# Kernel optimization log

Hardware: AMD Instinct MI355X
Metric: run time of the kernel (lower is better)

## Reference

```python
import jax, jax.numpy as jnp
import numpy as np

N = 50000
F_IN = 512
H = 256
L = 52
E = 1600000


def gcn_conv(x, W, b, src, dst):
    """PyG GCNConv: add self-loops, symmetric norm D^-1/2 (A+I) D^-1/2, then X W + b.
    src/dst already include self-loops."""
    h = x @ W  # [N, H]
    deg = jax.ops.segment_sum(jnp.ones_like(dst, dtype=h.dtype), dst, num_segments=N)
    dinv = jnp.where(deg > 0, jax.lax.rsqrt(deg), 0.0)
    w = dinv[src] * dinv[dst]  # [E+N]
    out = jax.ops.segment_sum(h[src] * w[:, None], dst, num_segments=N)
    return out + b


def _branch(x, src, dst, params):
    (W1, b1), (W2, b2), (W3, b3), (We, be) = params
    x = jax.nn.relu(gcn_conv(x, W1, b1, src, dst))
    x = jax.nn.relu(gcn_conv(x, W2, b2, src, dst))
    x = jax.nn.relu(gcn_conv(x, W3, b3, src, dst))
    return gcn_conv(x, We, be, src, dst)


def setup_inputs() -> dict:
    key = jax.random.key(0)
    ks = jax.random.split(key, 32)
    d = {}
    d["x_1"] = jax.random.normal(ks[0], (N, F_IN), dtype=jnp.float32)
    d["x_2"] = jax.random.normal(ks[1], (N, F_IN), dtype=jnp.float32)
    d["edge_index_1"] = jax.random.randint(ks[2], (2, E), 0, N, dtype=jnp.int32)
    d["edge_index_2"] = jax.random.randint(ks[3], (2, E), 0, N, dtype=jnp.int32)

    def lin(k, fi, fo):
        s = 1.0 / np.sqrt(fi)
        return jax.random.uniform(k, (fi, fo), jnp.float32, -s, s)

    i = 4
    for br in (1, 2):
        fis = [F_IN, H, H, H]
        for li, nm in enumerate(["1", "2", "3", "e"]):
            d[f"Wc{nm}{br}"] = lin(ks[i], fis[li], H); i += 1
            d[f"bc{nm}{br}"] = jnp.zeros((H,), jnp.float32)
    d["w1_W"] = lin(ks[i], H, 1); i += 1
    d["w1_b"] = jnp.zeros((1,), jnp.float32)
    d["w2_W"] = lin(ks[i], H, 1); i += 1
    d["w2_b"] = jnp.zeros((1,), jnp.float32)
    d["fin_W"] = lin(ks[i], H, H); i += 1
    d["fin_b"] = jnp.zeros((H,), jnp.float32)
    d["out_W"] = lin(ks[i], H, L); i += 1
    d["out_b"] = jnp.zeros((L,), jnp.float32)
    return d


def reference(x_1, edge_index_1, x_2, edge_index_2,
              Wc11, bc11, Wc21, bc21, Wc31, bc31, Wce1, bce1,
              Wc12, bc12, Wc22, bc22, Wc32, bc32, Wce2, bce2,
              w1_W, w1_b, w2_W, w2_b, fin_W, fin_b, out_W, out_b):
    loop = jnp.arange(N)
    s1 = jnp.concatenate([edge_index_1[0], loop])
    d1 = jnp.concatenate([edge_index_1[1], loop])
    s2 = jnp.concatenate([edge_index_2[0], loop])
    d2 = jnp.concatenate([edge_index_2[1], loop])

    h1 = _branch(x_1, s1, d1, [(Wc11, bc11), (Wc21, bc21), (Wc31, bc31), (Wce1, bce1)])
    h2 = _branch(x_2, s2, d2, [(Wc12, bc12), (Wc22, bc22), (Wc32, bc32), (Wce2, bce2)])

    f1 = jax.nn.sigmoid(h1 @ w1_W + w1_b)  # [N,1]
    f2 = jax.nn.sigmoid(h2 @ w2_W + w2_b)
    f1 = f1 / (f1 + f2)
    out = f1 * h1 + (1.0 - f1) * h2
    out = jax.nn.relu(out @ fin_W + fin_b)
    return jax.nn.sigmoid(out @ out_W + out_b)
```

## Files before the change

kernel.cpp:

```cpp
#include <hip/hip_runtime.h>
#include <math.h>

#define N_NODES 50000
#define F_IN    512
#define HDIM    256
#define L_OUT   52
#define E_EDGES 1600000

typedef short short8 __attribute__((ext_vector_type(8)));
typedef unsigned short u16x8 __attribute__((ext_vector_type(8)));
typedef float f32x4 __attribute__((ext_vector_type(4)));
typedef float f32x2 __attribute__((ext_vector_type(2)));

__device__ __forceinline__ float bf2f(unsigned short u) {
    unsigned int x = ((unsigned int)u) << 16;
    return __builtin_bit_cast(float, x);
}
__device__ __forceinline__ unsigned short f2bf(float f) {
    unsigned int u = __builtin_bit_cast(unsigned int, f);
    return (unsigned short)((u + 0x7fffu + ((u >> 16) & 1u)) >> 16);
}
__device__ __forceinline__ unsigned char f2fp8(float f) {
    int pk = __builtin_amdgcn_cvt_pk_fp8_f32(f, 0.f, 0, false);
    return (unsigned char)(pk & 0xff);
}
__device__ __forceinline__ void gload16(const unsigned short* g, unsigned short* l) {
    __builtin_amdgcn_global_load_lds(
        (const __attribute__((address_space(1))) unsigned int*)(g),
        (__attribute__((address_space(3))) unsigned int*)(l), 16, 0, 0);
}


__global__ void k_rank2(const int* __restrict__ d1, const int* __restrict__ d2,
                        int* __restrict__ c1, int* __restrict__ c2,
                        int* __restrict__ rk1, int* __restrict__ rk2, int E) {
    int i = blockIdx.x * blockDim.x + threadIdx.x;
    int stride = gridDim.x * blockDim.x;
    int tot = 2 * E;
    for (; i < tot; i += stride) {
        if (i < E) rk1[i] = atomicAdd(&c1[d1[i]], 1);
        else       rk2[i - E] = atomicAdd(&c2[d2[i - E]], 1);
    }
}

__global__ void k_dinv2(const int* __restrict__ c1, const int* __restrict__ c2,
                        float* __restrict__ v1, float* __restrict__ v2, int n) {
    int i = blockIdx.x * blockDim.x + threadIdx.x;
    if (i < n) v1[i] = rsqrtf((float)(c1[i] + 1));
    else if (i < 2 * n) v2[i - n] = rsqrtf((float)(c2[i - n] + 1));
}

__global__ void k_scan1f(const int* __restrict__ c1, const int* __restrict__ c2,
                         int* __restrict__ i1, int* __restrict__ i2,
                         int* __restrict__ b1, int* __restrict__ b2, int n) {
    const int* cnt = blockIdx.y ? c2 : c1;
    int* incl = blockIdx.y ? i2 : i1;
    int* bsum = blockIdx.y ? b2 : b1;
    __shared__ int s[256];
    int tid = threadIdx.x;
    int idx = blockIdx.x * 256 + tid;
    int v = (idx < n) ? cnt[idx] : 0;
    s[tid] = v;
    __syncthreads();
#pragma unroll
    for (int off = 1; off < 256; off <<= 1) {
        int t = (tid >= off) ? s[tid - off] : 0;
        __syncthreads();
        s[tid] += t;
        __syncthreads();
    }
    if (idx < n) incl[idx] = s[tid];
    if (tid == 255) bsum[blockIdx.x] = s[255];
}

__global__ void k_scan2f(int* __restrict__ b1, int* __restrict__ b2,
                         int* __restrict__ r1, int* __restrict__ r2, int nb, int n) {
    int* bsum = blockIdx.x ? b2 : b1;
    int* rowptr = blockIdx.x ? r2 : r1;
    __shared__ int s[256];
    int tid = threadIdx.x;
    int v = (tid < nb) ? bsum[tid] : 0;
    s[tid] = v;
    __syncthreads();
#pragma unroll
    for (int off = 1; off < 256; off <<= 1) {
        int t = (tid >= off) ? s[tid - off] : 0;
        __syncthreads();
        s[tid] += t;
        __syncthreads();
    }
    if (tid < nb) bsum[tid] = s[tid] - v;
    if (tid == nb - 1) rowptr[n] = s[tid];
}

__global__ void k_scan3f(const int* __restrict__ i1, const int* __restrict__ i2,
                         const int* __restrict__ c1, const int* __restrict__ c2,
                         const int* __restrict__ b1, const int* __restrict__ b2,
                         int* __restrict__ r1, int* __restrict__ r2, int n) {
    const int* incl = blockIdx.y ? i2 : i1;
    const int* cnt  = blockIdx.y ? c2 : c1;
    const int* bsum = blockIdx.y ? b2 : b1;
    int* rowptr     = blockIdx.y ? r2 : r1;
    int i = blockIdx.x * blockDim.x + threadIdx.x;
    if (i < n) rowptr[i] = incl[i] - cnt[i] + bsum[i >> 8];
}

__global__ void k_fill2(const int* __restrict__ s1, const int* __restrict__ d1,
                        const int* __restrict__ s2, const int* __restrict__ d2,
                        const int* __restrict__ rk1, const int* __restrict__ rk2,
                        const int* __restrict__ rp1, const int* __restrict__ rp2,
                        unsigned short* __restrict__ col1, unsigned short* __restrict__ col2,
                        int E) {
    int i = blockIdx.x * blockDim.x + threadIdx.x;
    int stride = gridDim.x * blockDim.x;
    int tot = 2 * E;
    for (; i < tot; i += stride) {
        int br = i >= E;
        int e = br ? i - E : i;
        const int* S = br ? s2 : s1;
        const int* D = br ? d2 : d1;
        const int* RK = br ? rk2 : rk1;
        const int* RP = br ? rp2 : rp1;
        unsigned short* C = br ? col2 : col1;
        int d = D[e];
        C[RP[d] + RK[e]] = (unsigned short)S[e];
    }
}


__global__ void k_f2b2(const float* __restrict__ x1, const float* __restrict__ x2,
                       unsigned short* __restrict__ o1, unsigned short* __restrict__ o2,
                       int n4) {
    int i = blockIdx.x * blockDim.x + threadIdx.x;
    int stride = gridDim.x * blockDim.x;
    int tot = 2 * n4;
    for (; i < tot; i += stride) {
        int br = i >= n4;
        int e = br ? i - n4 : i;
        float4 v = ((const float4*)(br ? x2 : x1))[e];
        ushort4 o;
        o.x = f2bf(v.x); o.y = f2bf(v.y); o.z = f2bf(v.z); o.w = f2bf(v.w);
        ((ushort4*)(br ? o2 : o1))[e] = o;
    }
}

struct WDesc { const float* in; unsigned short* out; int K; int N; int Npad; };
struct WPack { WDesc d[10]; };

__global__ void k_wconv(WPack p) {
    WDesc w = p.d[blockIdx.y];
    int total = w.K * w.Npad;
    int idx = blockIdx.x * 256 + threadIdx.x;
    if (idx >= total) return;
    int n = idx / w.K, k = idx - n * w.K;
    w.out[idx] = (n < w.N) ? f2bf(w.in[(size_t)k * w.N + n]) : (unsigned short)0;
}


__global__ void k_agg(const unsigned char* __restrict__ g, const int* __restrict__ rowptr,
                      const unsigned short* __restrict__ col,
                      const float* __restrict__ dinv,
                      const float* __restrict__ bias, unsigned short* __restrict__ out,
                      int n, int do_relu) {
    int gtid = blockIdx.x * blockDim.x + threadIdx.x;
    int wid = gtid >> 6;
    if (wid >= n) return;
    int lane = threadIdx.x & 63;
    int half = lane >> 5;
    int fl = lane & 31;

    float di = dinv[wid];

    float a[8];
#pragma unroll
    for (int k = 0; k < 8; k++) a[k] = 0.f;

    int r0 = rowptr[wid], r1 = rowptr[wid + 1];

    int base = r0;
    for (; base + 16 <= r1; base += 16) {
        int c[8]; float w[8]; uint2 v[8];
#pragma unroll
        for (int t = 0; t < 8; t++) c[t] = col[base + 2 * t + half];
#pragma unroll
        for (int t = 0; t < 8; t++) w[t] = dinv[c[t]];
#pragma unroll
        for (int t = 0; t < 8; t++)
            v[t] = ((const uint2*)(g + (size_t)c[t] * HDIM))[fl];
#pragma unroll
        for (int t = 0; t < 8; t++) {
            float wt = w[t] * di;
            f32x2 p0 = __builtin_amdgcn_cvt_pk_f32_fp8((int)v[t].x, false);
            f32x2 p1 = __builtin_amdgcn_cvt_pk_f32_fp8((int)v[t].x, true);
            f32x2 p2 = __builtin_amdgcn_cvt_pk_f32_fp8((int)v[t].y, false);
            f32x2 p3 = __builtin_amdgcn_cvt_pk_f32_fp8((int)v[t].y, true);
            a[0] = fmaf(p0[0], wt, a[0]); a[1] = fmaf(p0[1], wt, a[1]);
            a[2] = fmaf(p1[0], wt, a[2]); a[3] = fmaf(p1[1], wt, a[3]);
            a[4] = fmaf(p2[0], wt, a[4]); a[5] = fmaf(p2[1], wt, a[5]);
            a[6] = fmaf(p3[0], wt, a[6]); a[7] = fmaf(p3[1], wt, a[7]);
        }
    }
    if (base < r1) {
        int c[8]; float w[8]; uint2 v[8];
#pragma unroll
        for (int t = 0; t < 8; t++) {
            int idx = base + 2 * t + half;
            int ok = idx < r1;
            c[t] = col[ok ? idx : r0];
            w[t] = ok ? dinv[c[t]] : 0.f;
        }
#pragma unroll
        for (int t = 0; t < 8; t++)
            v[t] = ((const uint2*)(g + (size_t)c[t] * HDIM))[fl];
#pragma unroll
        for (int t = 0; t < 8; t++) {
            float wt = w[t] * di;
            f32x2 p0 = __builtin_amdgcn_cvt_pk_f32_fp8((int)v[t].x, false);
            f32x2 p1 = __builtin_amdgcn_cvt_pk_f32_fp8((int)v[t].x, true);
            f32x2 p2 = __builtin_amdgcn_cvt_pk_f32_fp8((int)v[t].y, false);
            f32x2 p3 = __builtin_amdgcn_cvt_pk_f32_fp8((int)v[t].y, true);
            a[0] = fmaf(p0[0], wt, a[0]); a[1] = fmaf(p0[1], wt, a[1]);
            a[2] = fmaf(p1[0], wt, a[2]); a[3] = fmaf(p1[1], wt, a[3]);
            a[4] = fmaf(p2[0], wt, a[4]); a[5] = fmaf(p2[1], wt, a[5]);
            a[6] = fmaf(p3[0], wt, a[6]); a[7] = fmaf(p3[1], wt, a[7]);
        }
    }

#pragma unroll
    for (int k = 0; k < 8; k++) a[k] += __shfl_xor(a[k], 32);

    float w0 = di * di;
    uint2 sv = ((const uint2*)(g + (size_t)wid * HDIM))[fl];
    f32x2 s0 = __builtin_amdgcn_cvt_pk_f32_fp8((int)sv.x, false);
    f32x2 s1 = __builtin_amdgcn_cvt_pk_f32_fp8((int)sv.x, true);
    f32x2 s2 = __builtin_amdgcn_cvt_pk_f32_fp8((int)sv.y, false);
    f32x2 s3 = __builtin_amdgcn_cvt_pk_f32_fp8((int)sv.y, true);
    float sf[8] = {s0[0], s0[1], s1[0], s1[1], s2[0], s2[1], s3[0], s3[1]};
    u16x8 o;
#pragma unroll
    for (int k = 0; k < 8; k++) {
        float x = fmaf(sf[k], w0, a[k]) + bias[fl * 8 + k];
        if (do_relu) x = fmaxf(x, 0.f);
        o[k] = f2bf(x);
    }
    if (half == 0)
        ((u16x8*)(out + (size_t)wid * HDIM))[fl] = o;
}


template <int EPI>
__global__ __launch_bounds__(256) void k_gemm(const unsigned short* __restrict__ A,
                                              const unsigned short* __restrict__ Bt,
                                              const float* __restrict__ bias,
                                              void* __restrict__ Cout,
                                              int M, int K, int Nc) {
    __shared__ __align__(16) unsigned short As[128 * 32];
    __shared__ __align__(16) unsigned short Bs[128 * 32];
    int tid = threadIdx.x;
    int wid = tid >> 6, lane = tid & 63;
    int wr = wid >> 1, wc = wid & 1;
    int mb = blockIdx.y * 128, nb = blockIdx.x * 128;

    int sr = tid >> 2;
    int ssl = (tid & 3) ^ ((sr >> 1) & 3);
    int ar0 = mb + sr;      if (ar0 > M - 1) ar0 = M - 1;
    int ar1 = mb + sr + 64; if (ar1 > M - 1) ar1 = M - 1;
    const unsigned short* gA0 = A + (size_t)ar0 * K + ssl * 8;
    const unsigned short* gA1 = A + (size_t)ar1 * K + ssl * 8;
    const unsigned short* gB0 = Bt + (size_t)(nb + sr) * K + ssl * 8;
    const unsigned short* gB1 = Bt + (size_t)(nb + sr + 64) * K + ssl * 8;
    unsigned short* ldsA = As + tid * 8;
    unsigned short* ldsB = Bs + tid * 8;

    f32x4 acc[4][4];
#pragma unroll
    for (int m = 0; m < 4; m++)
#pragma unroll
        for (int n = 0; n < 4; n++) acc[m][n] = (f32x4){0.f, 0.f, 0.f, 0.f};

    int l15 = lane & 15, ks = lane >> 4;

    for (int k0 = 0; k0 < K; k0 += 32) {
        gload16(gA0 + k0, ldsA);
        gload16(gA1 + k0, ldsA + 2048);
        gload16(gB0 + k0, ldsB);
        gload16(gB1 + k0, ldsB + 2048);
        __syncthreads();

        short8 af[4], bfr[4];
#pragma unroll
        for (int m = 0; m < 4; m++) {
            int row = wr * 64 + m * 16 + l15;
            int slot = ks ^ ((row >> 1) & 3);
            af[m] = *(const short8*)((const char*)As + row * 64 + slot * 16);
        }
#pragma unroll
        for (int n = 0; n < 4; n++) {
            int row = wc * 64 + n * 16 + l15;
            int slot = ks ^ ((row >> 1) & 3);
            bfr[n] = *(const short8*)((const char*)Bs + row * 64 + slot * 16);
        }
#pragma unroll
        for (int m = 0; m < 4; m++)
#pragma unroll
            for (int n = 0; n < 4; n++)
                acc[m][n] = __builtin_amdgcn_mfma_f32_16x16x32_bf16(af[m], bfr[n], acc[m][n], 0, 0, 0);
        __syncthreads();
    }

    int lq = lane >> 4;
#pragma unroll
    for (int m = 0; m < 4; m++) {
#pragma unroll
        for (int n = 0; n < 4; n++) {
            int gcol = nb + wc * 64 + n * 16 + l15;
#pragma unroll
            for (int r = 0; r < 4; r++) {
                int grow = mb + wr * 64 + m * 16 + lq * 4 + r;
                if (grow >= M) continue;
                float v = acc[m][n][r];
                if (EPI == 0) {
                    ((unsigned char*)Cout)[(size_t)grow * Nc + gcol] = f2fp8(v);
                } else if (EPI == 1) {
                    v += bias[gcol];
                    v = fmaxf(v, 0.f);
                    ((unsigned short*)Cout)[(size_t)grow * Nc + gcol] = f2bf(v);
                } else {
                    if (gcol < Nc) {
                        v += bias[gcol];
                        v = 1.f / (1.f + expf(-v));
                        ((float*)Cout)[(size_t)grow * Nc + gcol] = v;
                    }
                }
            }
        }
    }
}


__global__ void k_gate(const unsigned short* __restrict__ h1, const unsigned short* __restrict__ h2,
                       const float* __restrict__ w1, const float* __restrict__ w1b,
                       const float* __restrict__ w2, const float* __restrict__ w2b,
                       unsigned short* __restrict__ m, int n) {
    int gtid = blockIdx.x * blockDim.x + threadIdx.x;
    int wid = gtid >> 6;
    int lane = threadIdx.x & 63;
    if (wid >= n) return;
    ushort4 av = ((const ushort4*)(h1 + (size_t)wid * HDIM))[lane];
    ushort4 bv = ((const ushort4*)(h2 + (size_t)wid * HDIM))[lane];
    float4 wa = ((const float4*)w1)[lane];
    float4 wb = ((const float4*)w2)[lane];
    float a0 = bf2f(av.x), a1 = bf2f(av.y), a2 = bf2f(av.z), a3 = bf2f(av.w);
    float b0 = bf2f(bv.x), b1 = bf2f(bv.y), b2 = bf2f(bv.z), b3 = bf2f(bv.w);
    float d1 = a0 * wa.x + a1 * wa.y + a2 * wa.z + a3 * wa.w;
    float d2 = b0 * wb.x + b1 * wb.y + b2 * wb.z + b3 * wb.w;
    for (int off = 32; off > 0; off >>= 1) {
        d1 += __shfl_xor(d1, off);
        d2 += __shfl_xor(d2, off);
    }
    float f1 = 1.f / (1.f + expf(-(d1 + w1b[0])));
    float f2 = 1.f / (1.f + expf(-(d2 + w2b[0])));
    float f = f1 / (f1 + f2);
    ushort4 o;
    o.x = f2bf(f * a0 + (1.f - f) * b0);
    o.y = f2bf(f * a1 + (1.f - f) * b1);
    o.z = f2bf(f * a2 + (1.f - f) * b2);
    o.w = f2bf(f * a3 + (1.f - f) * b3);
    ((ushort4*)(m + (size_t)wid * HDIM))[lane] = o;
}


extern "C" void kernel_launch(void* const* d_in, const int* in_sizes, int n_in,
                              void* d_out, int out_size, void* d_ws, size_t ws_size,
                              hipStream_t stream) {
    (void)n_in; (void)out_size; (void)ws_size;
    const int N = N_NODES, E = E_EDGES;

    const float* x1; const float* x2; const int* ei1; const int* ei2;
    if (in_sizes[1] == 2 * E) {
        x1 = (const float*)d_in[0]; ei1 = (const int*)d_in[1];
        x2 = (const float*)d_in[2]; ei2 = (const int*)d_in[3];
    } else {
        x1 = (const float*)d_in[0]; x2 = (const float*)d_in[1];
        ei1 = (const int*)d_in[2]; ei2 = (const int*)d_in[3];
    }
    const float* W[2][4]; const float* Bv[2][4];
    int idx = 4;
    for (int br = 0; br < 2; br++)
        for (int l = 0; l < 4; l++) {
            W[br][l] = (const float*)d_in[idx++];
            Bv[br][l] = (const float*)d_in[idx++];
        }
    const float* w1W  = (const float*)d_in[20];
    const float* w1b  = (const float*)d_in[21];
    const float* w2W  = (const float*)d_in[22];
    const float* w2b  = (const float*)d_in[23];
    const float* finW = (const float*)d_in[24];
    const float* finb = (const float*)d_in[25];
    const float* outW = (const float*)d_in[26];
    const float* outb = (const float*)d_in[27];
    float* out = (float*)d_out;

    size_t off = 0;
    auto alloc = [&](size_t bytes) {
        void* p = (char*)d_ws + off;
        off = (off + bytes + 255) & ~(size_t)255;
        return p;
    };
    unsigned short* x1b = (unsigned short*)alloc((size_t)N * F_IN * 2);
    unsigned short* x2b = (unsigned short*)alloc((size_t)N * F_IN * 2);
    unsigned char*  g8  = (unsigned char*)alloc((size_t)N * HDIM);
    unsigned short* mb_ = (unsigned short*)alloc((size_t)N * HDIM * 2);
    unsigned short* h1b = (unsigned short*)alloc((size_t)N * HDIM * 2);
    unsigned short* h2b = (unsigned short*)alloc((size_t)N * HDIM * 2);
    unsigned short* Wt[2][4];
    Wt[0][0] = (unsigned short*)alloc((size_t)HDIM * F_IN * 2);
    for (int l = 1; l < 4; l++) Wt[0][l] = (unsigned short*)alloc((size_t)HDIM * HDIM * 2);
    Wt[1][0] = (unsigned short*)alloc((size_t)HDIM * F_IN * 2);
    for (int l = 1; l < 4; l++) Wt[1][l] = (unsigned short*)alloc((size_t)HDIM * HDIM * 2);
    unsigned short* finWt = (unsigned short*)alloc((size_t)HDIM * HDIM * 2);
    unsigned short* outWt = (unsigned short*)alloc((size_t)128 * HDIM * 2);
    unsigned short* col1 = (unsigned short*)alloc((size_t)E * 2);
    unsigned short* col2 = (unsigned short*)alloc((size_t)E * 2);
    int* rank1  = (int*)alloc((size_t)E * 4);
    int* rank2  = (int*)alloc((size_t)E * 4);
    int* rp1    = (int*)alloc((size_t)(N + 1) * 4);
    int* rp2    = (int*)alloc((size_t)(N + 1) * 4);
    int* incl1  = (int*)alloc((size_t)N * 4);
    int* incl2  = (int*)alloc((size_t)N * 4);
    int* bsum1  = (int*)alloc((size_t)256 * 4);
    int* bsum2  = (int*)alloc((size_t)256 * 4);
    int* cnt1   = (int*)alloc((size_t)N * 4);
    int* cnt2   = (int*)alloc((size_t)N * 4);
    float* di1  = (float*)alloc((size_t)N * 4);
    float* di2  = (float*)alloc((size_t)N * 4);

    const int BLK = 256;
    int nwaves_grid = (N * 64 + BLK - 1) / BLK;
    int nchunks = (N + 255) / 256;
    int mtiles = (N + 127) / 128;
    dim3 grid_h(HDIM / 128, mtiles);
    dim3 grid_o(1, mtiles);

    WPack wp;
    wp.d[0] = {W[0][0], Wt[0][0], F_IN, HDIM, HDIM};
    wp.d[1] = {W[0][1], Wt[0][1], HDIM, HDIM, HDIM};
    wp.d[2] = {W[0][2], Wt[0][2], HDIM, HDIM, HDIM};
    wp.d[3] = {W[0][3], Wt[0][3], HDIM, HDIM, HDIM};
    wp.d[4] = {W[1][0], Wt[1][0], F_IN, HDIM, HDIM};
    wp.d[5] = {W[1][1], Wt[1][1], HDIM, HDIM, HDIM};
    wp.d[6] = {W[1][2], Wt[1][2], HDIM, HDIM, HDIM};
    wp.d[7] = {W[1][3], Wt[1][3], HDIM, HDIM, HDIM};
    wp.d[8] = {finW, finWt, HDIM, HDIM, HDIM};
    wp.d[9] = {outW, outWt, HDIM, L_OUT, 128};
    k_wconv<<<dim3(512, 10), BLK, 0, stream>>>(wp);

    hipMemsetAsync(cnt1, 0, (size_t)N * 4, stream);
    hipMemsetAsync(cnt2, 0, (size_t)N * 4, stream);
    k_rank2<<<2048, BLK, 0, stream>>>(ei1 + E, ei2 + E, cnt1, cnt2, rank1, rank2, E);
    k_scan1f<<<dim3(nchunks, 2), BLK, 0, stream>>>(cnt1, cnt2, incl1, incl2, bsum1, bsum2, N);
    k_scan2f<<<2, BLK, 0, stream>>>(bsum1, bsum2, rp1, rp2, nchunks, N);
    k_scan3f<<<dim3(nchunks, 2), BLK, 0, stream>>>(incl1, incl2, cnt1, cnt2, bsum1, bsum2, rp1, rp2, N);
    k_dinv2<<<(2 * N + BLK - 1) / BLK, BLK, 0, stream>>>(cnt1, cnt2, di1, di2, N);
    k_fill2<<<4096, BLK, 0, stream>>>(ei1, ei1 + E, ei2, ei2 + E, rank1, rank2,
                                      rp1, rp2, col1, col2, E);
    k_f2b2<<<4096, BLK, 0, stream>>>(x1, x2, x1b, x2b, N * F_IN / 4);

    for (int br = 0; br < 2; br++) {
        const unsigned short* col = br ? col2 : col1;
        const int* rp = br ? rp2 : rp1;
        const float* di = br ? di2 : di1;
        const unsigned short* xb = br ? x2b : x1b;
        unsigned short* hb = br ? h2b : h1b;

        k_gemm<0><<<grid_h, BLK, 0, stream>>>(xb, Wt[br][0], nullptr, g8, N, F_IN, HDIM);
        k_agg<<<nwaves_grid, BLK, 0, stream>>>(g8, rp, col, di, Bv[br][0], hb, N, 1);
        for (int l = 1; l <= 2; l++) {
            k_gemm<0><<<grid_h, BLK, 0, stream>>>(hb, Wt[br][l], nullptr, g8, N, HDIM, HDIM);
            k_agg<<<nwaves_grid, BLK, 0, stream>>>(g8, rp, col, di, Bv[br][l], hb, N, 1);
        }
        k_gemm<0><<<grid_h, BLK, 0, stream>>>(hb, Wt[br][3], nullptr, g8, N, HDIM, HDIM);
        k_agg<<<nwaves_grid, BLK, 0, stream>>>(g8, rp, col, di, Bv[br][3], hb, N, 0);
    }

    k_gate<<<nwaves_grid, BLK, 0, stream>>>(h1b, h2b, w1W, w1b, w2W, w2b, mb_, N);
    k_gemm<1><<<grid_h, BLK, 0, stream>>>(mb_, finWt, finb, x1b, N, HDIM, HDIM);
    k_gemm<2><<<grid_o, BLK, 0, stream>>>(x1b, outWt, outb, out, N, HDIM, L_OUT);
}
```

Baseline: 1.029 ms.

## Replace atomic-rank CSR build with two-level bucket radix sort; unroll aggregation deeper

The CSR construction drops global atomic ranking and the three-pass scan. It now runs a two-level counting sort: per-block histograms over 128-node buckets in LDS, a scan, a scatter of packed (dst,src) records, and a per-bucket LDS sort that writes col, rowptr and counts. This is meant to remove contended global atomics and the random scatter writes. The aggregation kernel also gets a 32-edge unrolled loop for more memory-level parallelism, at the cost of more registers. Neighbour order within a row is now nondeterministic, and source ids are packed into 16 bits, which the earlier ushort col format already assumed.

Measured after the change: 892.6 us. 13.2% less time.

```diff
diff --git a/kernel.cpp b/kernel.cpp
--- a/kernel.cpp
+++ b/kernel.cpp
@@ -6,6 +6,9 @@
 #define HDIM    256
 #define L_OUT   52
 #define E_EDGES 1600000
+#define NB1     391
+#define EB      2048
+#define NBLK    782
 
 typedef short short8 __attribute__((ext_vector_type(8)));
 typedef unsigned short u16x8 __attribute__((ext_vector_type(8)));
@@ -31,17 +34,144 @@
 }
 
 
-__global__ void k_rank2(const int* __restrict__ d1, const int* __restrict__ d2,
-                        int* __restrict__ c1, int* __restrict__ c2,
-                        int* __restrict__ rk1, int* __restrict__ rk2, int E) {
-    int i = blockIdx.x * blockDim.x + threadIdx.x;
-    int stride = gridDim.x * blockDim.x;
-    int tot = 2 * E;
-    for (; i < tot; i += stride) {
-        if (i < E) rk1[i] = atomicAdd(&c1[d1[i]], 1);
-        else       rk2[i - E] = atomicAdd(&c2[d2[i - E]], 1);
-    }
-}
+__global__ __launch_bounds__(256) void k_hist(const int* __restrict__ d1, const int* __restrict__ d2,
+                                              int* __restrict__ h1, int* __restrict__ h2, int E) {
+    const int* D = blockIdx.y ? d2 : d1;
+    int* H = blockIdx.y ? h2 : h1;
+    __shared__ int h[NB1];
+    for (int t = threadIdx.x; t < NB1; t += 256) h[t] = 0;
+    __syncthreads();
+    int base = blockIdx.x * EB;
+#pragma unroll
+    for (int k = 0; k < 8; k++) {
+        int e = base + k * 256 + threadIdx.x;
+        if (e < E) atomicAdd(&h[D[e] >> 7], 1);
+    }
+    __syncthreads();
+    for (int t = threadIdx.x; t < NB1; t += 256)
+        H[(size_t)t * NBLK + blockIdx.x] = h[t];
+}
+
+__global__ __launch_bounds__(256) void k_scanb(int* __restrict__ h1, int* __restrict__ h2,
+                                               int* __restrict__ t1, int* __restrict__ t2) {
+    int* H = blockIdx.y ? h2 : h1;
+    int* T = blockIdx.y ? t2 : t1;
+    int b = blockIdx.x;
+    __shared__ int s[256];
+    int carry = 0;
+    for (int base = 0; base < NBLK; base += 256) {
+        int i = base + threadIdx.x;
+        int v = (i < NBLK) ? H[(size_t)b * NBLK + i] : 0;
+        s[threadIdx.x] = v;
+        __syncthreads();
+        for (int off = 1; off < 256; off <<= 1) {
+            int t = (threadIdx.x >= off) ? s[threadIdx.x - off] : 0;
+            __syncthreads();
+            s[threadIdx.x] += t;
+            __syncthreads();
+        }
+        if (i < NBLK) H[(size_t)b * NBLK + i] = carry + s[threadIdx.x] - v;
+        int ct = s[255];
+        __syncthreads();
+        carry += ct;
+    }
+    if (threadIdx.x == 0) T[b] = carry;
+}
+
+__global__ __launch_bounds__(512) void k_bstart(const int* __restrict__ t1, const int* __restrict__ t2,
+                                                int* __restrict__ b1, int* __restrict__ b2,
+                                                int* __restrict__ rp1, int* __restrict__ rp2,
+                                                int N, int E) {
+    const int* T = blockIdx.y ? t2 : t1;
+    int* BS = blockIdx.y ? b2 : b1;
+    int* RP = blockIdx.y ? rp2 : rp1;
+    __shared__ int s[512];
+    int v = (threadIdx.x < NB1) ? T[threadIdx.x] : 0;
+    s[threadIdx.x] = v;
+    __syncthreads();
+    for (int off = 1; off < 512; off <<= 1) {
+        int t = (threadIdx.x >= off) ? s[threadIdx.x - off] : 0;
+        __syncthreads();
+        s[threadIdx.x] += t;
+        __syncthreads();
+    }
+    if (threadIdx.x < NB1) BS[threadIdx.x] = s[threadIdx.x] - v;
+    if (threadIdx.x == 0) { BS[NB1] = E; RP[N] = E; }
+}
+
+__global__ __launch_bounds__(256) void k_scatter(const int* __restrict__ s1, const int* __restrict__ d1,
+                                                 const int* __restrict__ s2, const int* __restrict__ d2,
+                                                 const int* __restrict__ h1, const int* __restrict__ h2,
+                                                 const int* __restrict__ b1, const int* __restrict__ b2,
+                                                 unsigned int* __restrict__ r1, unsigned int* __restrict__ r2,
+                                                 int E) {
+    int br = blockIdx.y;
+    const int* S = br ? s2 : s1;
+    const int* D = br ? d2 : d1;
+    const int* H = br ? h2 : h1;
+    const int* BS = br ? b2 : b1;
+    unsigned int* R = br ? r2 : r1;
+    __shared__ int cur[NB1];
+    for (int t = threadIdx.x; t < NB1; t += 256)
+        cur[t] = BS[t] + H[(size_t)t * NBLK + blockIdx.x];
+    __syncthreads();
+    int base = blockIdx.x * EB;
+#pragma unroll
+    for (int k = 0; k < 8; k++) {
+        int e = base + k * 256 + threadIdx.x;
+        if (e < E) {
+            int d = D[e];
+            int p = atomicAdd(&cur[d >> 7], 1);
+            R[p] = (unsigned int)(S[e] & 0xFFFF) | ((unsigned int)d << 16);
+        }
+    }
+}
+
+__global__ __launch_bounds__(256) void k_sort(const unsigned int* __restrict__ r1,
+                                              const unsigned int* __restrict__ r2,
+                                              const int* __restrict__ b1, const int* __restrict__ b2,
+                                              int* __restrict__ c1, int* __restrict__ c2,
+                                              int* __restrict__ rp1, int* __restrict__ rp2,
+                                              unsigned short* __restrict__ col1,
+                                              unsigned short* __restrict__ col2, int N) {
+    int br = blockIdx.y;
+    const unsigned int* R = br ? r2 : r1;
+    const int* BS = br ? b2 : b1;
+    int* CNT = br ? c2 : c1;
+    int* RP = br ? rp2 : rp1;
+    unsigned short* COL = br ? col2 : col1;
+    int b = blockIdx.x;
+    int s = BS[b], sz = BS[b + 1] - s;
+    __shared__ int h[128], sc[128], cur[128];
+    if (threadIdx.x < 128) h[threadIdx.x] = 0;
+    __syncthreads();
+    for (int i = s + threadIdx.x; i < s + sz; i += 256)
+        atomicAdd(&h[(R[i] >> 16) & 127], 1);
+    __syncthreads();
+    if (threadIdx.x < 128) sc[threadIdx.x] = h[threadIdx.x];
+    __syncthreads();
+    for (int off = 1; off < 128; off <<= 1) {
+        int t = 0;
+        if (threadIdx.x < 128 && threadIdx.x >= off) t = sc[threadIdx.x - off];
+        __syncthreads();
+        if (threadIdx.x < 128) sc[threadIdx.x] += t;
+        __syncthreads();
+    }
+    if (threadIdx.x < 128) {
+        int excl = sc[threadIdx.x] - h[threadIdx.x];
+        cur[threadIdx.x] = excl;
+        int node = b * 128 + threadIdx.x;
+        if (node < N) { CNT[node] = h[threadIdx.x]; RP[node] = s + excl; }
+    }
+    __syncthreads();
+    for (int i = s + threadIdx.x; i < s + sz; i += 256) {
+        unsigned int r = R[i];
+        int low = (r >> 16) & 127;
+        int p = atomicAdd(&cur[low], 1);
+        COL[s + p] = (unsigned short)(r & 0xFFFFu);
+    }
+}
+
 
 __global__ void k_dinv2(const int* __restrict__ c1, const int* __restrict__ c2,
                         float* __restrict__ v1, float* __restrict__ v2, int n) {
@@ -49,84 +179,6 @@
     if (i < n) v1[i] = rsqrtf((float)(c1[i] + 1));
     else if (i < 2 * n) v2[i - n] = rsqrtf((float)(c2[i - n] + 1));
 }
-
-__global__ void k_scan1f(const int* __restrict__ c1, const int* __restrict__ c2,
-                         int* __restrict__ i1, int* __restrict__ i2,
-                         int* __restrict__ b1, int* __restrict__ b2, int n) {
-    const int* cnt = blockIdx.y ? c2 : c1;
-    int* incl = blockIdx.y ? i2 : i1;
-    int* bsum = blockIdx.y ? b2 : b1;
-    __shared__ int s[256];
-    int tid = threadIdx.x;
-    int idx = blockIdx.x * 256 + tid;
-    int v = (idx < n) ? cnt[idx] : 0;
-    s[tid] = v;
-    __syncthreads();
-#pragma unroll
-    for (int off = 1; off < 256; off <<= 1) {
-        int t = (tid >= off) ? s[tid - off] : 0;
-        __syncthreads();
-        s[tid] += t;
-        __syncthreads();
-    }
-    if (idx < n) incl[idx] = s[tid];
-    if (tid == 255) bsum[blockIdx.x] = s[255];
-}
-
-__global__ void k_scan2f(int* __restrict__ b1, int* __restrict__ b2,
-                         int* __restrict__ r1, int* __restrict__ r2, int nb, int n) {
-    int* bsum = blockIdx.x ? b2 : b1;
-    int* rowptr = blockIdx.x ? r2 : r1;
-    __shared__ int s[256];
-    int tid = threadIdx.x;
-    int v = (tid < nb) ? bsum[tid] : 0;
-    s[tid] = v;
-    __syncthreads();
-#pragma unroll
-    for (int off = 1; off < 256; off <<= 1) {
-        int t = (tid >= off) ? s[tid - off] : 0;
-        __syncthreads();
-        s[tid] += t;
-        __syncthreads();
-    }
-    if (tid < nb) bsum[tid] = s[tid] - v;
-    if (tid == nb - 1) rowptr[n] = s[tid];
-}
-
-__global__ void k_scan3f(const int* __restrict__ i1, const int* __restrict__ i2,
-                         const int* __restrict__ c1, const int* __restrict__ c2,
-                         const int* __restrict__ b1, const int* __restrict__ b2,
-                         int* __restrict__ r1, int* __restrict__ r2, int n) {
-    const int* incl = blockIdx.y ? i2 : i1;
-    const int* cnt  = blockIdx.y ? c2 : c1;
-    const int* bsum = blockIdx.y ? b2 : b1;
-    int* rowptr     = blockIdx.y ? r2 : r1;
-    int i = blockIdx.x * blockDim.x + threadIdx.x;
-    if (i < n) rowptr[i] = incl[i] - cnt[i] + bsum[i >> 8];
-}
-
-__global__ void k_fill2(const int* __restrict__ s1, const int* __restrict__ d1,
-                        const int* __restrict__ s2, const int* __restrict__ d2,
-                        const int* __restrict__ rk1, const int* __restrict__ rk2,
-                        const int* __restrict__ rp1, const int* __restrict__ rp2,
-                        unsigned short* __restrict__ col1, unsigned short* __restrict__ col2,
-                        int E) {
-    int i = blockIdx.x * blockDim.x + threadIdx.x;
-    int stride = gridDim.x * blockDim.x;
-    int tot = 2 * E;
-    for (; i < tot; i += stride) {
-        int br = i >= E;
-        int e = br ? i - E : i;
-        const int* S = br ? s2 : s1;
-        const int* D = br ? d2 : d1;
-        const int* RK = br ? rk2 : rk1;
-        const int* RP = br ? rp2 : rp1;
-        unsigned short* C = br ? col2 : col1;
-        int d = D[e];
-        C[RP[d] + RK[e]] = (unsigned short)S[e];
-    }
-}
-
 
 __global__ void k_f2b2(const float* __restrict__ x1, const float* __restrict__ x2,
                        unsigned short* __restrict__ o1, unsigned short* __restrict__ o2,
@@ -176,8 +228,30 @@
     for (int k = 0; k < 8; k++) a[k] = 0.f;
 
     int r0 = rowptr[wid], r1 = rowptr[wid + 1];
-
     int base = r0;
+
+    for (; base + 32 <= r1; base += 32) {
+        int c[16]; float w[16]; uint2 v[16];
+#pragma unroll
+        for (int t = 0; t < 16; t++) c[t] = col[base + 2 * t + half];
+#pragma unroll
+        for (int t = 0; t < 16; t++) w[t] = dinv[c[t]];
+#pragma unroll
+        for (int t = 0; t < 16; t++)
+            v[t] = ((const uint2*)(g + (size_t)c[t] * HDIM))[fl];
+#pragma unroll
+        for (int t = 0; t < 16; t++) {
+            float wt = w[t] * di;
+            f32x2 p0 = __builtin_amdgcn_cvt_pk_f32_fp8((int)v[t].x, false);
+            f32x2 p1 = __builtin_amdgcn_cvt_pk_f32_fp8((int)v[t].x, true);
+            f32x2 p2 = __builtin_amdgcn_cvt_pk_f32_fp8((int)v[t].y, false);
+            f32x2 p3 = __builtin_amdgcn_cvt_pk_f32_fp8((int)v[t].y, true);
+            a[0] = fmaf(p0[0], wt, a[0]); a[1] = fmaf(p0[1], wt, a[1]);
+            a[2] = fmaf(p1[0], wt, a[2]); a[3] = fmaf(p1[1], wt, a[3]);
+            a[4] = fmaf(p2[0], wt, a[4]); a[5] = fmaf(p2[1], wt, a[5]);
+            a[6] = fmaf(p3[0], wt, a[6]); a[7] = fmaf(p3[1], wt, a[7]);
+        }
+    }
     for (; base + 16 <= r1; base += 16) {
         int c[8]; float w[8]; uint2 v[8];
 #pragma unroll
@@ -422,14 +496,16 @@
     unsigned short* outWt = (unsigned short*)alloc((size_t)128 * HDIM * 2);
     unsigned short* col1 = (unsigned short*)alloc((size_t)E * 2);
     unsigned short* col2 = (unsigned short*)alloc((size_t)E * 2);
-    int* rank1  = (int*)alloc((size_t)E * 4);
-    int* rank2  = (int*)alloc((size_t)E * 4);
+    unsigned int* rec1 = (unsigned int*)alloc((size_t)E * 4);
+    unsigned int* rec2 = (unsigned int*)alloc((size_t)E * 4);
+    int* hist1  = (int*)alloc((size_t)NB1 * NBLK * 4);
+    int* hist2  = (int*)alloc((size_t)NB1 * NBLK * 4);
+    int* tot1   = (int*)alloc((size_t)NB1 * 4);
+    int* tot2   = (int*)alloc((size_t)NB1 * 4);
+    int* bs1    = (int*)alloc((size_t)(NB1 + 1) * 4);
+    int* bs2    = (int*)alloc((size_t)(NB1 + 1) * 4);
     int* rp1    = (int*)alloc((size_t)(N + 1) * 4);
     int* rp2    = (int*)alloc((size_t)(N + 1) * 4);
-    int* incl1  = (int*)alloc((size_t)N * 4);
-    int* incl2  = (int*)alloc((size_t)N * 4);
-    int* bsum1  = (int*)alloc((size_t)256 * 4);
-    int* bsum2  = (int*)alloc((size_t)256 * 4);
     int* cnt1   = (int*)alloc((size_t)N * 4);
     int* cnt2   = (int*)alloc((size_t)N * 4);
     float* di1  = (float*)alloc((size_t)N * 4);
@@ -437,7 +513,6 @@
 
     const int BLK = 256;
     int nwaves_grid = (N * 64 + BLK - 1) / BLK;
-    int nchunks = (N + 255) / 256;
     int mtiles = (N + 127) / 128;
     dim3 grid_h(HDIM / 128, mtiles);
     dim3 grid_o(1, mtiles);
@@ -454,17 +529,16 @@
     wp.d[8] = {finW, finWt, HDIM, HDIM, HDIM};
     wp.d[9] = {outW, outWt, HDIM, L_OUT, 128};
     k_wconv<<<dim3(512, 10), BLK, 0, stream>>>(wp);
-
-    hipMemsetAsync(cnt1, 0, (size_t)N * 4, stream);
-    hipMemsetAsync(cnt2, 0, (size_t)N * 4, stream);
-    k_rank2<<<2048, BLK, 0, stream>>>(ei1 + E, ei2 + E, cnt1, cnt2, rank1, rank2, E);
-    k_scan1f<<<dim3(nchunks, 2), BLK, 0, stream>>>(cnt1, cnt2, incl1, incl2, bsum1, bsum2, N);
-    k_scan2f<<<2, BLK, 0, stream>>>(bsum1, bsum2, rp1, rp2, nchunks, N);
-    k_scan3f<<<dim3(nchunks, 2), BLK, 0, stream>>>(incl1, incl2, cnt1, cnt2, bsum1, bsum2, rp1, rp2, N);
+    k_f2b2<<<4096, BLK, 0, stream>>>(x1, x2, x1b, x2b, N * F_IN / 4);
+
+    k_hist<<<dim3(NBLK, 2), BLK, 0, stream>>>(ei1 + E, ei2 + E, hist1, hist2, E);
+    k_scanb<<<dim3(NB1, 2), BLK, 0, stream>>>(hist1, hist2, tot1, tot2);
+    k_bstart<<<dim3(1, 2), 512, 0, stream>>>(tot1, tot2, bs1, bs2, rp1, rp2, N, E);
+    k_scatter<<<dim3(NBLK, 2), BLK, 0, stream>>>(ei1, ei1 + E, ei2, ei2 + E,
+                                                 hist1, hist2, bs1, bs2, rec1, rec2, E);
+    k_sort<<<dim3(NB1, 2), BLK, 0, stream>>>(rec1, rec2, bs1, bs2,
+                                             cnt1, cnt2, rp1, rp2, col1, col2, N);
     k_dinv2<<<(2 * N + BLK - 1) / BLK, BLK, 0, stream>>>(cnt1, cnt2, di1, di2, N);
-    k_fill2<<<4096, BLK, 0, stream>>>(ei1, ei1 + E, ei2, ei2 + E, rank1, rank2,
-                                      rp1, rp2, col1, col2, E);
-    k_f2b2<<<4096, BLK, 0, stream>>>(x1, x2, x1b, x2b, N * F_IN / 4);
 
     for (int br = 0; br < 2; br++) {
         const unsigned short* col = br ? col2 : col1;
```
